# Performance work log

Measured on AMD Instinct MI355X. Metric: run time of the kernel, lower is better.

Reference implementation:

```python
import jax, jax.numpy as jnp
import numpy as np

D_K = 64

def setup_inputs() -> dict:
    key = jax.random.key(0)
    kx, kq, kk, kv = jax.random.split(key, 4)
    B, T, D = 4, 2048, 1024
    s = 1.0 / np.sqrt(D)
    return {
        "x": jax.random.normal(kx, (B, T, D), dtype=jnp.float32),
        "Wq": jax.random.normal(kq, (D, D_K), dtype=jnp.float32) * s,
        "Wk": jax.random.normal(kk, (D, D_K), dtype=jnp.float32) * s,
        "Wv": jax.random.normal(kv, (D, D_K), dtype=jnp.float32) * s,
    }

def reference(x, Wq, Wk, Wv):
    # x: [B, T, D]; Wq/Wk/Wv: [D, d_k]
    Q = x @ Wq  # [B, T, d_k]
    K = x @ Wk
    V = x @ Wv
    scale = 1.0 / jnp.sqrt(jnp.asarray(Q.shape[-1], Q.dtype))
    scores = jnp.einsum('btd,bsd->bts', Q, K) * scale  # [B, T, T]
    T = scores.shape[-1]
    causal = jnp.tril(jnp.ones((T, T), dtype=bool))  # keep lower-tri incl diag
    masked = jnp.where(causal, scores, -jnp.inf)
    attn = jax.nn.softmax(masked, axis=-1)  # dropout p=0.0 -> identity
    context = jnp.einsum('bts,bsd->btd', attn, V)  # [B, T, d_k]
    return context
```

## Files before the change

### kernel.cpp

```cpp
#include <hip/hip_runtime.h>
#include <math.h>

#define BT    8192
#define TSEQ  2048
#define DIN   1024
#define DK    64

typedef __attribute__((ext_vector_type(8))) short bf16x8;
typedef __attribute__((ext_vector_type(4))) short bf16x4;
typedef __attribute__((ext_vector_type(4))) float f32x4;

static __device__ inline unsigned short f2bf(float f) {
    union { float f; unsigned u; } v; v.f = f;
    unsigned r = v.u + 0x7fff + ((v.u >> 16) & 1);
    return (unsigned short)(r >> 16);
}

static __device__ inline bf16x4 cvt4(float4 a) {
    bf16x4 r;
    r[0] = (short)f2bf(a.x); r[1] = (short)f2bf(a.y);
    r[2] = (short)f2bf(a.z); r[3] = (short)f2bf(a.w);
    return r;
}

__global__ __launch_bounds__(256) void wt_kernel(
    const float* __restrict__ Wq, const float* __restrict__ Wk,
    const float* __restrict__ Wv, unsigned short* __restrict__ WT)
{
    __shared__ float ws[64][65];
    const int tid = threadIdx.x;
    const int mat = blockIdx.x >> 4;
    const int k0  = (blockIdx.x & 15) << 6;
    const float* W = (mat == 0) ? Wq : ((mat == 1) ? Wk : Wv);

    const int j = tid & 63;
    for (int i = tid >> 6; i < 64; i += 4)
        ws[i][j] = W[(size_t)(k0 + i) * DK + j];
    __syncthreads();

    const int n  = tid & 63;
    const int c0 = (tid >> 6) << 4;
    unsigned short* dst = WT + (size_t)(mat * 64 + n) * DIN + k0 + c0;
    #pragma unroll
    for (int c = 0; c < 16; ++c) dst[c] = f2bf(ws[c0 + c][n]);
}

__global__ __launch_bounds__(256, 2) void proj_kernel(
    const float* __restrict__ x, const unsigned short* __restrict__ WT,
    unsigned short* __restrict__ Qb, unsigned short* __restrict__ Kb,
    unsigned short* __restrict__ VT)
{
    __shared__ unsigned short xs[16][1032];
    __shared__ unsigned short wtb[192][72];
    const int tid = threadIdx.x;
    const int m0 = blockIdx.x * 16;

    {
        const int r = tid >> 4;
        const int c = (tid & 15) << 2;
        const float* src = x + (size_t)(m0 + r) * DIN + c;
        float4 tmp[16];
        #pragma unroll
        for (int s = 0; s < 16; ++s) tmp[s] = *(const float4*)(src + s * 64);
        #pragma unroll
        for (int s = 0; s < 16; ++s) *(bf16x4*)&xs[r][c + s * 64] = cvt4(tmp[s]);
    }

    const int lane = tid & 63;
    const int w    = tid >> 6;
    const int lr = lane & 15, lg = lane >> 4;

    f32x4 acc[3];
    #pragma unroll
    for (int nt = 0; nt < 3; ++nt) acc[nt] = (f32x4){0.f, 0.f, 0.f, 0.f};

    const unsigned short* wt_w = WT + (size_t)w * 48 * DIN;
    bf16x8 cur[6], nxt[6];
    #pragma unroll
    for (int i = 0; i < 6; ++i) {
        const int c = lane + i * 64;
        const int nl = c >> 3;
        const int sl = c & 7;
        cur[i] = *(const bf16x8*)(wt_w + (size_t)nl * DIN + (sl << 3));
    }

    __syncthreads();

    for (int kc = 0; kc < 16; ++kc) {
        const int k0 = kc << 6;

        if (kc + 1 < 16) {
            #pragma unroll
            for (int i = 0; i < 6; ++i) {
                const int c = lane + i * 64;
                const int nl = c >> 3;
                const int sl = c & 7;
                nxt[i] = *(const bf16x8*)(wt_w + (size_t)nl * DIN
                                          + (k0 + 64) + (sl << 3));
            }
        }

        #pragma unroll
        for (int i = 0; i < 6; ++i) {
            const int c = lane + i * 64;
            const int n = w * 48 + (c >> 3);
            const int sl = c & 7;
            *(bf16x8*)&wtb[n][((sl + n) & 7) << 3] = cur[i];
        }
        asm volatile("s_waitcnt lgkmcnt(0)" ::: "memory");

        #pragma unroll
        for (int st = 0; st < 2; ++st) {
            const bf16x8 af = *(const bf16x8*)&xs[lr][k0 + (st << 5) + (lg << 3)];
            #pragma unroll
            for (int nt = 0; nt < 3; ++nt) {
                const int n = w * 48 + nt * 16 + lr;
                const int sl = (st << 2) + lg;
                const bf16x8 bf = *(const bf16x8*)&wtb[n][((sl + n) & 7) << 3];
                acc[nt] = __builtin_amdgcn_mfma_f32_16x16x32_bf16(af, bf, acc[nt], 0, 0, 0);
            }
        }

        if (kc + 1 < 16) {
            #pragma unroll
            for (int i = 0; i < 6; ++i) cur[i] = nxt[i];
        }
    }

    const float qsc = 0.125f * 1.44269504088896340736f;
    #pragma unroll
    for (int nt = 0; nt < 3; ++nt) {
        const int gct = w * 3 + nt;
        if (gct < 8) {
            #pragma unroll
            for (int r = 0; r < 4; ++r) {
                const int row = m0 + (lg << 2) + r;
                const float vv = acc[nt][r];
                if (gct < 4) Qb[(size_t)row * DK + gct * 16 + lr] = f2bf(vv * qsc);
                else         Kb[(size_t)row * DK + (gct - 4) * 16 + lr] = f2bf(vv);
            }
        } else {
            const int d = (gct - 8) * 16 + lr;
            const int t = m0 + (lg << 2);
            ushort4 pk;
            pk.x = f2bf(acc[nt][0]); pk.y = f2bf(acc[nt][1]);
            pk.z = f2bf(acc[nt][2]); pk.w = f2bf(acc[nt][3]);
            *(ushort4*)&VT[((size_t)(t >> 11) * DK + d) * TSEQ + (t & (TSEQ - 1))] = pk;
        }
    }
}

__global__ __launch_bounds__(256, 2) void attn_kernel(
    const unsigned short* __restrict__ Qb, const unsigned short* __restrict__ Kb,
    const unsigned short* __restrict__ VT, float* __restrict__ O)
{
    __shared__ __align__(16) unsigned short P_lds[4][16][72];
    __shared__ float Opart[4][16][68];
    __shared__ float mpart[4][16];
    __shared__ float Lpart[4][16];

    const int lane = threadIdx.x & 63;
    const int w    = threadIdx.x >> 6;
    const int qt = ((blockIdx.x & 3) << 7) | (127 - (blockIdx.x >> 2));
    const int q0 = qt << 4;
    const int t0 = q0 & (TSEQ - 1);
    const int b  = q0 >> 11;
    const int lr = lane & 15;
    const int lg = lane >> 4;

    const unsigned short* Qrow = Qb + (size_t)(q0 + lr) * DK + (lg << 3);
    const bf16x8 qf0 = *(const bf16x8*)(Qrow);
    const bf16x8 qf1 = *(const bf16x8*)(Qrow + 32);

    const unsigned short* Kbase = Kb + (size_t)b * TSEQ * DK;
    const unsigned short* Vbase = VT + (size_t)b * DK * TSEQ;

    f32x4 oacc[4];
    #pragma unroll
    for (int dt = 0; dt < 4; ++dt) oacc[dt] = (f32x4){0.f, 0.f, 0.f, 0.f};
    float m[4] = {-INFINITY, -INFINITY, -INFINITY, -INFINITY};
    float L[4] = {0.f, 0.f, 0.f, 0.f};

    const int nkb = (t0 >> 6) + 1;

    bf16x8 kf0[4], kf1[4];
    if (w < nkb) {
        const int s0 = w << 6;
        #pragma unroll
        for (int ct = 0; ct < 4; ++ct) {
            const unsigned short* Krow =
                Kbase + (size_t)(s0 + ct * 16 + lr) * DK + (lg << 3);
            kf0[ct] = *(const bf16x8*)(Krow);
            kf1[ct] = *(const bf16x8*)(Krow + 32);
        }
    }

    for (int kb = w; kb < nkb; kb += 4) {
        const int s0 = kb << 6;

        f32x4 s[4];
        #pragma unroll
        for (int ct = 0; ct < 4; ++ct) {
            f32x4 a = (f32x4){0.f, 0.f, 0.f, 0.f};
            a = __builtin_amdgcn_mfma_f32_16x16x32_bf16(qf0, kf0[ct], a, 0, 0, 0);
            a = __builtin_amdgcn_mfma_f32_16x16x32_bf16(qf1, kf1[ct], a, 0, 0, 0);
            s[ct] = a;
        }

        bf16x8 vf0[4], vf1[4];
        #pragma unroll
        for (int dt = 0; dt < 4; ++dt) {
            const unsigned short* Vrow =
                Vbase + (size_t)(dt * 16 + lr) * TSEQ + s0 + (lg << 3);
            vf0[dt] = *(const bf16x8*)(Vrow);
            vf1[dt] = *(const bf16x8*)(Vrow + 32);
        }

        bf16x8 nk0[4], nk1[4];
        if (kb + 4 < nkb) {
            const int sn = (kb + 4) << 6;
            #pragma unroll
            for (int ct = 0; ct < 4; ++ct) {
                const unsigned short* Krow =
                    Kbase + (size_t)(sn + ct * 16 + lr) * DK + (lg << 3);
                nk0[ct] = *(const bf16x8*)(Krow);
                nk1[ct] = *(const bf16x8*)(Krow + 32);
            }
        }

        if (kb == nkb - 1) {
            #pragma unroll
            for (int ct = 0; ct < 4; ++ct)
                #pragma unroll
                for (int r = 0; r < 4; ++r)
                    if (s0 + ct * 16 + lr > t0 + lg * 4 + r) s[ct][r] = -INFINITY;
        }

        float pm[4];
        #pragma unroll
        for (int r = 0; r < 4; ++r)
            pm[r] = fmaxf(fmaxf(s[0][r], s[1][r]), fmaxf(s[2][r], s[3][r]));

        bool near = true;
        #pragma unroll
        for (int r = 0; r < 4; ++r)
            near = near && (pm[r] - m[r] <= 8.0f);

        if (!__all(near)) {
            float tmax[4];
            #pragma unroll
            for (int r = 0; r < 4; ++r) tmax[r] = pm[r];
            #pragma unroll
            for (int off = 1; off < 16; off <<= 1)
                #pragma unroll
                for (int r = 0; r < 4; ++r)
                    tmax[r] = fmaxf(tmax[r], __shfl_xor(tmax[r], off));

            float f[4];
            #pragma unroll
            for (int r = 0; r < 4; ++r) {
                const float mn = fmaxf(m[r], tmax[r]);
                f[r] = exp2f(m[r] - mn);
                m[r] = mn;
            }
            #pragma unroll
            for (int r = 0; r < 4; ++r) L[r] *= f[r];
            #pragma unroll
            for (int r = 0; r < 4; ++r) {
                oacc[0][r] *= f[r]; oacc[1][r] *= f[r];
                oacc[2][r] *= f[r]; oacc[3][r] *= f[r];
            }
        }

        float ps[4] = {0.f, 0.f, 0.f, 0.f};
        unsigned short pb[4][4];
        #pragma unroll
        for (int ct = 0; ct < 4; ++ct)
            #pragma unroll
            for (int r = 0; r < 4; ++r) {
                const float p = exp2f(s[ct][r] - m[r]);
                ps[r] += p;
                pb[ct][r] = f2bf(p);
            }
        #pragma unroll
        for (int r = 0; r < 4; ++r) L[r] += ps[r];

        #pragma unroll
        for (int ct = 0; ct < 4; ++ct)
            #pragma unroll
            for (int r = 0; r < 4; ++r)
                P_lds[w][lg * 4 + r][ct * 16 + lr] = pb[ct][r];
        asm volatile("s_waitcnt lgkmcnt(0)" ::: "memory");
        const bf16x8 pf0 = *(const bf16x8*)&P_lds[w][lr][(lg << 3)];
        const bf16x8 pf1 = *(const bf16x8*)&P_lds[w][lr][32 + (lg << 3)];

        #pragma unroll
        for (int dt = 0; dt < 4; ++dt) {
            oacc[dt] = __builtin_amdgcn_mfma_f32_16x16x32_bf16(pf0, vf0[dt], oacc[dt], 0, 0, 0);
            oacc[dt] = __builtin_amdgcn_mfma_f32_16x16x32_bf16(pf1, vf1[dt], oacc[dt], 0, 0, 0);
        }

        #pragma unroll
        for (int ct = 0; ct < 4; ++ct) { kf0[ct] = nk0[ct]; kf1[ct] = nk1[ct]; }
    }

    #pragma unroll
    for (int off = 1; off < 16; off <<= 1)
        #pragma unroll
        for (int r = 0; r < 4; ++r) L[r] += __shfl_xor(L[r], off);

    #pragma unroll
    for (int dt = 0; dt < 4; ++dt)
        #pragma unroll
        for (int r = 0; r < 4; ++r)
            Opart[w][(lg << 2) + r][dt * 16 + lr] = oacc[dt][r];
    if (lr == 0) {
        #pragma unroll
        for (int r = 0; r < 4; ++r) {
            mpart[w][(lg << 2) + r] = m[r];
            Lpart[w][(lg << 2) + r] = L[r];
        }
    }
    __syncthreads();

    #pragma unroll
    for (int r = 0; r < 4; ++r) {
        const int row = (lg << 2) + r;
        const float M = fmaxf(fmaxf(mpart[0][row], mpart[1][row]),
                              fmaxf(mpart[2][row], mpart[3][row]));
        float Lf = 0.f, o = 0.f;
        #pragma unroll
        for (int v = 0; v < 4; ++v) {
            const float fv = exp2f(mpart[v][row] - M);
            Lf += fv * Lpart[v][row];
            o  += fv * Opart[v][row][(w << 4) + lr];
        }
        O[(size_t)(q0 + row) * DK + (w << 4) + lr] = o / Lf;
    }
}

extern "C" void kernel_launch(void* const* d_in, const int* in_sizes, int n_in,
                              void* d_out, int out_size, void* d_ws, size_t ws_size,
                              hipStream_t stream) {
    const float* x  = (const float*)d_in[0];
    const float* Wq = (const float*)d_in[1];
    const float* Wk = (const float*)d_in[2];
    const float* Wv = (const float*)d_in[3];
    float* O = (float*)d_out;

    unsigned short* Qb = (unsigned short*)d_ws;
    unsigned short* Kb = Qb + (size_t)BT * DK;
    unsigned short* VT = Kb + (size_t)BT * DK;
    unsigned short* WT = VT + (size_t)BT * DK;

    wt_kernel  <<<dim3(48),  dim3(256), 0, stream>>>(Wq, Wk, Wv, WT);
    proj_kernel<<<dim3(512), dim3(256), 0, stream>>>(x, WT, Qb, Kb, VT);
    attn_kernel<<<dim3(512), dim3(256), 0, stream>>>(Qb, Kb, VT, O);
}
```

Measured before the change: 47.91 us.

## Stage K/V tiles in shared memory with double buffering across query tiles

Restructures the attention kernel so each block handles 32 queries (two 16-row tiles) and cooperatively loads 128-key K/V chunks into swizzled, double-buffered LDS. The two wave pairs share those chunks, so K/V global reads are shared across waves instead of each wave reading its own fragments. V is stored in 64-column tiles by the projection kernel to make the staged loads contiguous. The merge scratch is unioned with the K/V buffers. Grid size halves to 256 and launch bounds drop to one block per CU, which lowers parallelism and adds a block-wide barrier every iteration. The causal split is uneven, since waves with h=1 skip the last half chunk.

```diff
diff --git a/kernel.cpp b/kernel.cpp
--- a/kernel.cpp
+++ b/kernel.cpp
@@ -142,38 +142,47 @@
         } else {
             const int d = (gct - 8) * 16 + lr;
             const int t = m0 + (lg << 2);
+            const int tb = t & (TSEQ - 1);
+            const size_t tile = (size_t)(t >> 11) * 32 + (tb >> 6);
             ushort4 pk;
             pk.x = f2bf(acc[nt][0]); pk.y = f2bf(acc[nt][1]);
             pk.z = f2bf(acc[nt][2]); pk.w = f2bf(acc[nt][3]);
-            *(ushort4*)&VT[((size_t)(t >> 11) * DK + d) * TSEQ + (t & (TSEQ - 1))] = pk;
-        }
-    }
-}
-
-__global__ __launch_bounds__(256, 2) void attn_kernel(
+            *(ushort4*)&VT[(tile * DK + d) * 64 + (tb & 63)] = pk;
+        }
+    }
+}
+
+__global__ __launch_bounds__(256, 1) void attn_kernel(
     const unsigned short* __restrict__ Qb, const unsigned short* __restrict__ Kb,
     const unsigned short* __restrict__ VT, float* __restrict__ O)
 {
+    union __align__(16) Sh {
+        struct { unsigned short K[2][128][64]; unsigned short V[2][2][64][64]; } kv;
+        struct { float Op[4][16][68]; float mp[4][16]; float Lp[4][16]; } mg;
+    };
+    __shared__ Sh sh;
     __shared__ __align__(16) unsigned short P_lds[4][16][72];
-    __shared__ float Opart[4][16][68];
-    __shared__ float mpart[4][16];
-    __shared__ float Lpart[4][16];
-
-    const int lane = threadIdx.x & 63;
-    const int w    = threadIdx.x >> 6;
-    const int qt = ((blockIdx.x & 3) << 7) | (127 - (blockIdx.x >> 2));
-    const int q0 = qt << 4;
-    const int t0 = q0 & (TSEQ - 1);
-    const int b  = q0 >> 11;
-    const int lr = lane & 15;
-    const int lg = lane >> 4;
-
-    const unsigned short* Qrow = Qb + (size_t)(q0 + lr) * DK + (lg << 3);
+
+    const int tid  = threadIdx.x;
+    const int lane = tid & 63;
+    const int w    = tid >> 6;
+    const int t    = w >> 1;
+    const int h    = w & 1;
+    const int bi   = blockIdx.x;
+    const int batch = bi & 3;
+    const int jj   = bi >> 2;
+    const int t0   = jj << 5;
+    const int t_first = t0 + (t << 4);
+    const int t_last  = t_first + 15;
+    const int q0t  = (batch << 11) + t_first;
+    const int lr = lane & 15, lg = lane >> 4;
+
+    const unsigned short* Qrow = Qb + (size_t)(q0t + lr) * DK + (lg << 3);
     const bf16x8 qf0 = *(const bf16x8*)(Qrow);
     const bf16x8 qf1 = *(const bf16x8*)(Qrow + 32);
 
-    const unsigned short* Kbase = Kb + (size_t)b * TSEQ * DK;
-    const unsigned short* Vbase = VT + (size_t)b * DK * TSEQ;
+    const unsigned short* Kbase = Kb + (size_t)batch * TSEQ * DK;
+    const unsigned short* Vbase = VT + (size_t)batch * 32 * DK * 64;
 
     f32x4 oacc[4];
     #pragma unroll
@@ -181,162 +190,160 @@
     float m[4] = {-INFINITY, -INFINITY, -INFINITY, -INFINITY};
     float L[4] = {0.f, 0.f, 0.f, 0.f};
 
-    const int nkb = (t0 >> 6) + 1;
-
-    bf16x8 kf0[4], kf1[4];
-    if (w < nkb) {
-        const int s0 = w << 6;
-        #pragma unroll
-        for (int ct = 0; ct < 4; ++ct) {
-            const unsigned short* Krow =
-                Kbase + (size_t)(s0 + ct * 16 + lr) * DK + (lg << 3);
-            kf0[ct] = *(const bf16x8*)(Krow);
-            kf1[ct] = *(const bf16x8*)(Krow + 32);
-        }
-    }
-
-    for (int kb = w; kb < nkb; kb += 4) {
-        const int s0 = kb << 6;
-
-        f32x4 s[4];
-        #pragma unroll
-        for (int ct = 0; ct < 4; ++ct) {
-            f32x4 a = (f32x4){0.f, 0.f, 0.f, 0.f};
-            a = __builtin_amdgcn_mfma_f32_16x16x32_bf16(qf0, kf0[ct], a, 0, 0, 0);
-            a = __builtin_amdgcn_mfma_f32_16x16x32_bf16(qf1, kf1[ct], a, 0, 0, 0);
-            s[ct] = a;
-        }
-
-        bf16x8 vf0[4], vf1[4];
-        #pragma unroll
-        for (int dt = 0; dt < 4; ++dt) {
-            const unsigned short* Vrow =
-                Vbase + (size_t)(dt * 16 + lr) * TSEQ + s0 + (lg << 3);
-            vf0[dt] = *(const bf16x8*)(Vrow);
-            vf1[dt] = *(const bf16x8*)(Vrow + 32);
-        }
-
-        bf16x8 nk0[4], nk1[4];
-        if (kb + 4 < nkb) {
-            const int sn = (kb + 4) << 6;
+    const int nkb2 = ((t0 + 31) >> 7) + 1;
+
+#define STAGE_LOAD(C2) do {                                                   \
+    const unsigned short* ksrc_ = Kbase + ((size_t)(C2) << 13);               \
+    const unsigned short* vsrc_ = Vbase + ((size_t)(C2) << 13);               \
+    _Pragma("unroll")                                                         \
+    for (int ld_ = 0; ld_ < 4; ++ld_) {                                       \
+        kst[ld_] = *(const bf16x8*)(ksrc_ + (((ld_ << 8) + tid) << 3));       \
+        vst[ld_] = *(const bf16x8*)(vsrc_ + (((ld_ << 8) + tid) << 3));       \
+    }                                                                         \
+} while (0)
+
+#define STAGE_WRITE(B) do {                                                   \
+    _Pragma("unroll")                                                         \
+    for (int ld_ = 0; ld_ < 4; ++ld_) {                                       \
+        const int c_ = (ld_ << 8) + tid;                         \
+        const int rk_ = c_ >> 3, slk_ = c_ & 7;                               \
+        *(bf16x8*)&sh.kv.K[B][rk_][((slk_ ^ (rk_ & 7)) << 3)] = kst[ld_];     \
+        const int jv_ = c_ >> 9, cc_ = c_ & 511;                              \
+        const int rv_ = cc_ >> 3, slv_ = cc_ & 7;                             \
+        *(bf16x8*)&sh.kv.V[B][jv_][rv_][((slv_ ^ (rv_ & 7)) << 3)] = vst[ld_];\
+    }                                                                         \
+} while (0)
+
+    bf16x8 kst[4], vst[4];
+    STAGE_LOAD(0);
+    STAGE_WRITE(0);
+    __syncthreads();
+
+    for (int i2 = 0; i2 < nkb2; ++i2) {
+        const int curb = i2 & 1;
+
+        if (i2 + 1 < nkb2) STAGE_LOAD(i2 + 1);
+
+        const int s0 = (i2 << 7) + (h << 6);
+        if (s0 <= t_last) {
+            f32x4 s[4];
             #pragma unroll
             for (int ct = 0; ct < 4; ++ct) {
-                const unsigned short* Krow =
-                    Kbase + (size_t)(sn + ct * 16 + lr) * DK + (lg << 3);
-                nk0[ct] = *(const bf16x8*)(Krow);
-                nk1[ct] = *(const bf16x8*)(Krow + 32);
-            }
-        }
-
-        if (kb == nkb - 1) {
+                const int row = (h << 6) + ct * 16 + lr;
+                const bf16x8 k0 = *(const bf16x8*)&sh.kv.K[curb][row][((lg ^ (row & 7)) << 3)];
+                const bf16x8 k1 = *(const bf16x8*)&sh.kv.K[curb][row][(((lg + 4) ^ (row & 7)) << 3)];
+                f32x4 a = (f32x4){0.f, 0.f, 0.f, 0.f};
+                a = __builtin_amdgcn_mfma_f32_16x16x32_bf16(qf0, k0, a, 0, 0, 0);
+                a = __builtin_amdgcn_mfma_f32_16x16x32_bf16(qf1, k1, a, 0, 0, 0);
+                s[ct] = a;
+            }
+
+            if (s0 + 63 > t_first) {
+                #pragma unroll
+                for (int ct = 0; ct < 4; ++ct)
+                    #pragma unroll
+                    for (int r = 0; r < 4; ++r)
+                        if (s0 + ct * 16 + lr > t_first + lg * 4 + r) s[ct][r] = -INFINITY;
+            }
+
+            float pm[4];
+            #pragma unroll
+            for (int r = 0; r < 4; ++r)
+                pm[r] = fmaxf(fmaxf(s[0][r], s[1][r]), fmaxf(s[2][r], s[3][r]));
+            bool near = true;
+            #pragma unroll
+            for (int r = 0; r < 4; ++r) near = near && (pm[r] - m[r] <= 8.0f);
+            if (!__all(near)) {
+                float tmax[4];
+                #pragma unroll
+                for (int r = 0; r < 4; ++r) tmax[r] = pm[r];
+                #pragma unroll
+                for (int off = 1; off < 16; off <<= 1)
+                    #pragma unroll
+                    for (int r = 0; r < 4; ++r)
+                        tmax[r] = fmaxf(tmax[r], __shfl_xor(tmax[r], off));
+                #pragma unroll
+                for (int r = 0; r < 4; ++r) {
+                    const float mn = fmaxf(m[r], tmax[r]);
+                    const float f = exp2f(m[r] - mn);
+                    m[r] = mn; L[r] *= f;
+                    oacc[0][r] *= f; oacc[1][r] *= f;
+                    oacc[2][r] *= f; oacc[3][r] *= f;
+                }
+            }
+            float ps[4] = {0.f, 0.f, 0.f, 0.f};
+            unsigned short pb[4][4];
             #pragma unroll
             for (int ct = 0; ct < 4; ++ct)
                 #pragma unroll
+                for (int r = 0; r < 4; ++r) {
+                    const float p = exp2f(s[ct][r] - m[r]);
+                    ps[r] += p;
+                    pb[ct][r] = f2bf(p);
+                }
+            #pragma unroll
+            for (int r = 0; r < 4; ++r) L[r] += ps[r];
+
+            #pragma unroll
+            for (int ct = 0; ct < 4; ++ct)
+                #pragma unroll
                 for (int r = 0; r < 4; ++r)
-                    if (s0 + ct * 16 + lr > t0 + lg * 4 + r) s[ct][r] = -INFINITY;
-        }
-
-        float pm[4];
+                    P_lds[w][lg * 4 + r][ct * 16 + lr] = pb[ct][r];
+            asm volatile("s_waitcnt lgkmcnt(0)" ::: "memory");
+            const bf16x8 pf0 = *(const bf16x8*)&P_lds[w][lr][(lg << 3)];
+            const bf16x8 pf1 = *(const bf16x8*)&P_lds[w][lr][32 + (lg << 3)];
+
+            #pragma unroll
+            for (int dt = 0; dt < 4; ++dt) {
+                const int rr = dt * 16 + lr;
+                const bf16x8 v0 = *(const bf16x8*)&sh.kv.V[curb][h][rr][((lg ^ (rr & 7)) << 3)];
+                const bf16x8 v1 = *(const bf16x8*)&sh.kv.V[curb][h][rr][(((lg + 4) ^ (rr & 7)) << 3)];
+                oacc[dt] = __builtin_amdgcn_mfma_f32_16x16x32_bf16(pf0, v0, oacc[dt], 0, 0, 0);
+                oacc[dt] = __builtin_amdgcn_mfma_f32_16x16x32_bf16(pf1, v1, oacc[dt], 0, 0, 0);
+            }
+        }
+
+        if (i2 + 1 < nkb2) STAGE_WRITE(curb ^ 1);
+        __syncthreads();
+    }
+
+    #pragma unroll
+    for (int off = 1; off < 16; off <<= 1)
+        #pragma unroll
+        for (int r = 0; r < 4; ++r) L[r] += __shfl_xor(L[r], off);
+
+    #pragma unroll
+    for (int dt = 0; dt < 4; ++dt)
         #pragma unroll
         for (int r = 0; r < 4; ++r)
-            pm[r] = fmaxf(fmaxf(s[0][r], s[1][r]), fmaxf(s[2][r], s[3][r]));
-
-        bool near = true;
-        #pragma unroll
-        for (int r = 0; r < 4; ++r)
-            near = near && (pm[r] - m[r] <= 8.0f);
-
-        if (!__all(near)) {
-            float tmax[4];
-            #pragma unroll
-            for (int r = 0; r < 4; ++r) tmax[r] = pm[r];
-            #pragma unroll
-            for (int off = 1; off < 16; off <<= 1)
-                #pragma unroll
-                for (int r = 0; r < 4; ++r)
-                    tmax[r] = fmaxf(tmax[r], __shfl_xor(tmax[r], off));
-
-            float f[4];
-            #pragma unroll
-            for (int r = 0; r < 4; ++r) {
-                const float mn = fmaxf(m[r], tmax[r]);
-                f[r] = exp2f(m[r] - mn);
-                m[r] = mn;
-            }
-            #pragma unroll
-            for (int r = 0; r < 4; ++r) L[r] *= f[r];
-            #pragma unroll
-            for (int r = 0; r < 4; ++r) {
-                oacc[0][r] *= f[r]; oacc[1][r] *= f[r];
-                oacc[2][r] *= f[r]; oacc[3][r] *= f[r];
-            }
-        }
-
-        float ps[4] = {0.f, 0.f, 0.f, 0.f};
-        unsigned short pb[4][4];
-        #pragma unroll
-        for (int ct = 0; ct < 4; ++ct)
-            #pragma unroll
-            for (int r = 0; r < 4; ++r) {
-                const float p = exp2f(s[ct][r] - m[r]);
-                ps[r] += p;
-                pb[ct][r] = f2bf(p);
-            }
-        #pragma unroll
-        for (int r = 0; r < 4; ++r) L[r] += ps[r];
-
-        #pragma unroll
-        for (int ct = 0; ct < 4; ++ct)
-            #pragma unroll
-            for (int r = 0; r < 4; ++r)
-                P_lds[w][lg * 4 + r][ct * 16 + lr] = pb[ct][r];
-        asm volatile("s_waitcnt lgkmcnt(0)" ::: "memory");
-        const bf16x8 pf0 = *(const bf16x8*)&P_lds[w][lr][(lg << 3)];
-        const bf16x8 pf1 = *(const bf16x8*)&P_lds[w][lr][32 + (lg << 3)];
-
-        #pragma unroll
-        for (int dt = 0; dt < 4; ++dt) {
-            oacc[dt] = __builtin_amdgcn_mfma_f32_16x16x32_bf16(pf0, vf0[dt], oacc[dt], 0, 0, 0);
-            oacc[dt] = __builtin_amdgcn_mfma_f32_16x16x32_bf16(pf1, vf1[dt], oacc[dt], 0, 0, 0);
-        }
-
-        #pragma unroll
-        for (int ct = 0; ct < 4; ++ct) { kf0[ct] = nk0[ct]; kf1[ct] = nk1[ct]; }
-    }
-
-    #pragma unroll
-    for (int off = 1; off < 16; off <<= 1)
-        #pragma unroll
-        for (int r = 0; r < 4; ++r) L[r] += __shfl_xor(L[r], off);
-
-    #pragma unroll
-    for (int dt = 0; dt < 4; ++dt)
-        #pragma unroll
-        for (int r = 0; r < 4; ++r)
-            Opart[w][(lg << 2) + r][dt * 16 + lr] = oacc[dt][r];
+            sh.mg.Op[w][(lg << 2) + r][dt * 16 + lr] = oacc[dt][r];
     if (lr == 0) {
         #pragma unroll
         for (int r = 0; r < 4; ++r) {
-            mpart[w][(lg << 2) + r] = m[r];
-            Lpart[w][(lg << 2) + r] = L[r];
+            sh.mg.mp[w][(lg << 2) + r] = m[r];
+            sh.mg.Lp[w][(lg << 2) + r] = L[r];
         }
     }
     __syncthreads();
 
-    #pragma unroll
-    for (int r = 0; r < 4; ++r) {
-        const int row = (lg << 2) + r;
-        const float M = fmaxf(fmaxf(mpart[0][row], mpart[1][row]),
-                              fmaxf(mpart[2][row], mpart[3][row]));
-        float Lf = 0.f, o = 0.f;
-        #pragma unroll
-        for (int v = 0; v < 4; ++v) {
-            const float fv = exp2f(mpart[v][row] - M);
-            Lf += fv * Lpart[v][row];
-            o  += fv * Opart[v][row][(w << 4) + lr];
-        }
-        O[(size_t)(q0 + row) * DK + (w << 4) + lr] = o / Lf;
-    }
+    const int v0 = t << 1, v1 = v0 + 1;
+    #pragma unroll
+    for (int c2 = 0; c2 < 2; ++c2) {
+        const int ctn = (h << 1) + c2;
+        #pragma unroll
+        for (int r = 0; r < 4; ++r) {
+            const int row = (lg << 2) + r;
+            const float M = fmaxf(sh.mg.mp[v0][row], sh.mg.mp[v1][row]);
+            const float f0 = exp2f(sh.mg.mp[v0][row] - M);
+            const float f1 = exp2f(sh.mg.mp[v1][row] - M);
+            const float Lf = f0 * sh.mg.Lp[v0][row] + f1 * sh.mg.Lp[v1][row];
+            const float o  = f0 * sh.mg.Op[v0][row][(ctn << 4) + lr]
+                           + f1 * sh.mg.Op[v1][row][(ctn << 4) + lr];
+            O[(size_t)(q0t + row) * DK + (ctn << 4) + lr] = o / Lf;
+        }
+    }
+#undef STAGE_LOAD
+#undef STAGE_WRITE
 }
 
 extern "C" void kernel_launch(void* const* d_in, const int* in_sizes, int n_in,
@@ -355,5 +362,5 @@
 
     wt_kernel  <<<dim3(48),  dim3(256), 0, stream>>>(Wq, Wk, Wv, WT);
     proj_kernel<<<dim3(512), dim3(256), 0, stream>>>(x, WT, Qb, Kb, VT);
-    attn_kernel<<<dim3(512), dim3(256), 0, stream>>>(Qb, Kb, VT, O);
-}
+    attn_kernel<<<dim3(256), dim3(256), 0, stream>>>(Qb, Kb, VT, O);
+}
```

Measured after the change: 52.31 us. +9.2%, slower.
